# Optimization experiments

Measured on AMD Instinct MI355X. Metric: run time of the kernel, lower is better.

Reference implementation:

```python
import jax, jax.numpy as jnp
import numpy as np

EOS = 1e-10
N = 6000          # nnodes
E = 192000        # n_edges (avg degree 32)
D_IN = 512        # input_dim
H = 128           # hidden_dim
ALPHA = 1.0
TEMP = 1.0
BIAS = 1e-4


def setup_inputs() -> dict:
    key = jax.random.key(0)
    k1, k2, k3, k4, k5, k6, k7 = jax.random.split(key, 7)
    features = jax.random.normal(k1, (N, D_IN), dtype=jnp.float32)
    edges = jax.random.randint(k2, (2, E), 0, N)
    # params: embedding Linear(D_IN->H) and edge MLP Linear(2H->1)
    w_emb = jax.random.normal(k3, (D_IN, H), dtype=jnp.float32) * 0.05
    b_emb = jnp.zeros((H,), jnp.float32)
    w_mlp = jax.random.normal(k4, (2 * H, 1), dtype=jnp.float32) * 0.05
    b_mlp = jnp.zeros((1,), jnp.float32)
    # gumbel-sigmoid noise: eps = (bias-(1-bias))*u + (1-bias)  in [bias, 1-bias]
    u = jax.random.uniform(k5, (E,), dtype=jnp.float32)
    eps = (BIAS - (1.0 - BIAS)) * u + (1.0 - BIAS)
    gate_noise = jnp.log(eps) - jnp.log(1.0 - eps)
    return {"features": features, "edges": edges, "w_emb": w_emb, "b_emb": b_emb,
            "w_mlp": w_mlp, "b_mlp": b_mlp, "gate_noise": gate_noise}


def _normalize_sym(adj):
    d = adj.sum(axis=1)
    inv = 1.0 / (jnp.sqrt(d) + EOS)
    return adj * inv[:, None] * inv[None, :]


def reference(features, edges, w_emb, b_emb, w_mlp, b_mlp, gate_noise):
    # node embeddings: single Linear + ReLU
    emb = jax.nn.relu(features @ w_emb + b_emb)              # [N, H]
    h0 = emb[edges[0]]                                       # [E, H]
    h1 = emb[edges[1]]                                       # [E, H]
    s1 = (jnp.concatenate([h0, h1], axis=1) @ w_mlp + b_mlp).ravel()
    s2 = (jnp.concatenate([h1, h0], axis=1) @ w_mlp + b_mlp).ravel()
    raw = (s1 + s2) * 0.5                                    # [E]
    # gumbel-sigmoid gating
    weights_lp = jax.nn.sigmoid((gate_noise + raw) / TEMP)
    weights_hp = 1.0 - weights_lp

    eye = jnp.eye(N, dtype=features.dtype)

    def build_adj(w):
        adj = jnp.zeros((N, N), features.dtype).at[edges[0], edges[1]].set(w)
        return _normalize_sym(adj + eye)

    adj_lp = build_adj(weights_lp)
    adj_hp = build_adj(weights_hp)
    mask = jnp.zeros((N, N), features.dtype).at[edges[0], edges[1]].set(1.0)
    adj_hp = eye - adj_hp * mask * ALPHA
    adj_unnorm = jnp.zeros((N, N), features.dtype).at[edges[0], edges[1]].set(1.0)
    return (adj_lp, adj_hp, weights_lp, weights_hp, adj_unnorm)
```

## Files before the change

### kernel.cpp

```cpp
#include <hip/hip_runtime.h>
#include <math.h>

#define NNODES 6000
#define NEDGES 192000
#define DIN 512
#define HDIM 128
#define ALPHA 1.0f
#define EOS 1e-10f

static const size_t NN = (size_t)NNODES * (size_t)NNODES;

__global__ __launch_bounds__(128) void embed_g_kernel(
    const float* __restrict__ feat, const float* __restrict__ w_emb,
    const float* __restrict__ b_emb, const float* __restrict__ w_mlp,
    float* __restrict__ g) {
  __shared__ float sf[8 * DIN];
  __shared__ float red[2][8];
  const int t = threadIdx.x;
  const int nb = blockIdx.x * 8;

  const float4* f4 = (const float4*)(feat + (size_t)nb * DIN);
  float4* s4 = (float4*)sf;
#pragma unroll
  for (int k = 0; k < 8; ++k) s4[k * 128 + t] = f4[k * 128 + t];
  __syncthreads();

  const int h = t;
  float acc[8];
  const float b = b_emb[h];
#pragma unroll
  for (int n = 0; n < 8; ++n) acc[n] = b;

#pragma unroll 4
  for (int d = 0; d < DIN; ++d) {
    const float w = w_emb[d * HDIM + h];
#pragma unroll
    for (int n = 0; n < 8; ++n) acc[n] += sf[n * DIN + d] * w;
  }

  const float wv = 0.5f * (w_mlp[h] + w_mlp[HDIM + h]);
  const int lane = t & 63, wave = t >> 6;
#pragma unroll
  for (int n = 0; n < 8; ++n) {
    float v = fmaxf(acc[n], 0.0f) * wv;
    for (int off = 32; off > 0; off >>= 1) v += __shfl_down(v, off, 64);
    if (lane == 0) red[wave][n] = v;
  }
  __syncthreads();
  if (t < 8) g[nb + t] = red[0][t] + red[1][t];
}

__global__ __launch_bounds__(256) void edge_weights_kernel(
    const int* __restrict__ edges, const float* __restrict__ g,
    const float* __restrict__ noise, const float* __restrict__ b_mlp,
    float* __restrict__ w_lp, float* __restrict__ w_hp,
    int* __restrict__ winner) {
  const int e = blockIdx.x * blockDim.x + threadIdx.x;
  if (e >= NEDGES) return;
  const int u = edges[e];
  const int v = edges[NEDGES + e];
  const float raw = g[u] + g[v] + b_mlp[0];
  const float x = noise[e] + raw;
  const float wl = 1.0f / (1.0f + expf(-x));
  const float wh = 1.0f - wl;
  w_lp[e] = wl;
  w_hp[e] = wh;
  atomicMax(&winner[(size_t)u * NNODES + v], e + 1);
}

__global__ __launch_bounds__(256) void edge_deg_kernel(
    const int* __restrict__ edges, const float* __restrict__ w_lp,
    const float* __restrict__ w_hp, const int* __restrict__ winner,
    float* __restrict__ deg_lp, float* __restrict__ deg_hp) {
  const int e = blockIdx.x * blockDim.x + threadIdx.x;
  if (e >= NEDGES) return;
  const int u = edges[e];
  const int v = edges[NEDGES + e];
  if (winner[(size_t)u * NNODES + v] != e + 1) return;
  atomicAdd(&deg_lp[u], w_lp[e]);
  atomicAdd(&deg_hp[u], w_hp[e]);
}

__global__ __launch_bounds__(256) void node_inv_kernel(
    const float* __restrict__ deg_lp, const float* __restrict__ deg_hp,
    float* __restrict__ inv_lp, float* __restrict__ inv_hp,
    float* __restrict__ adj_lp, float* __restrict__ adj_hp) {
  const int i = blockIdx.x * blockDim.x + threadIdx.x;
  if (i >= NNODES) return;
  const float il = 1.0f / (sqrtf(deg_lp[i] + 1.0f) + EOS);
  const float ih = 1.0f / (sqrtf(deg_hp[i] + 1.0f) + EOS);
  inv_lp[i] = il;
  inv_hp[i] = ih;
  const size_t diag = (size_t)i * NNODES + i;
  adj_lp[diag] = il * il;
  adj_hp[diag] = 1.0f;
}

__global__ __launch_bounds__(256) void edge_write_kernel(
    const int* __restrict__ edges, const float* __restrict__ w_lp,
    const float* __restrict__ w_hp, const float* __restrict__ inv_lp,
    const float* __restrict__ inv_hp, float* __restrict__ adj_lp,
    float* __restrict__ adj_hp, float* __restrict__ unnorm) {
  const int e = blockIdx.x * blockDim.x + threadIdx.x;
  if (e >= NEDGES) return;
  const int u = edges[e];
  const int v = edges[NEDGES + e];
  const size_t cell = (size_t)u * NNODES + v;
  const int win = ((const int*)unnorm)[cell];
  if (win != e + 1) return;
  const float wl = w_lp[e];
  const float wh = w_hp[e];
  const float il = inv_lp[u] * inv_lp[v];
  const float ih = inv_hp[u] * inv_hp[v];
  if (u == v) {
    adj_lp[cell] = (wl + 1.0f) * il;
    adj_hp[cell] = 1.0f - (wh + 1.0f) * ih * ALPHA;
  } else {
    adj_lp[cell] = wl * il;
    adj_hp[cell] = -wh * ih * ALPHA;
  }
  unnorm[cell] = 1.0f;
}

extern "C" void kernel_launch(void* const* d_in, const int* in_sizes, int n_in,
                              void* d_out, int out_size, void* d_ws,
                              size_t ws_size, hipStream_t stream) {
  const float* feat  = (const float*)d_in[0];
  const int*   edges = (const int*)d_in[1];
  const float* w_emb = (const float*)d_in[2];
  const float* b_emb = (const float*)d_in[3];
  const float* w_mlp = (const float*)d_in[4];
  const float* b_mlp = (const float*)d_in[5];
  const float* noise = (const float*)d_in[6];

  float* out    = (float*)d_out;
  float* adj_lp = out;
  float* adj_hp = out + NN;
  float* w_lp   = out + 2 * NN;
  float* w_hp   = w_lp + NEDGES;
  float* unnorm = w_hp + NEDGES;

  float* deg_lp = (float*)d_ws;
  float* deg_hp = deg_lp + NNODES;
  float* inv_lp = deg_hp + NNODES;
  float* inv_hp = inv_lp + NNODES;
  float* g      = inv_hp + NNODES;

  hipMemsetAsync(adj_lp, 0, 2 * NN * sizeof(float), stream);
  hipMemsetAsync(unnorm, 0, NN * sizeof(float), stream);
  hipMemsetAsync(deg_lp, 0, 2 * NNODES * sizeof(float), stream);

  embed_g_kernel<<<NNODES / 8, 128, 0, stream>>>(feat, w_emb, b_emb, w_mlp, g);

  const int eb = (NEDGES + 255) / 256;
  edge_weights_kernel<<<eb, 256, 0, stream>>>(edges, g, noise, b_mlp, w_lp,
                                              w_hp, (int*)unnorm);
  edge_deg_kernel<<<eb, 256, 0, stream>>>(edges, w_lp, w_hp,
                                          (const int*)unnorm, deg_lp, deg_hp);
  node_inv_kernel<<<(NNODES + 255) / 256, 256, 0, stream>>>(
      deg_lp, deg_hp, inv_lp, inv_hp, adj_lp, adj_hp);
  edge_write_kernel<<<eb, 256, 0, stream>>>(edges, w_lp, w_hp, inv_lp, inv_hp,
                                            adj_lp, adj_hp, unnorm);
}
```

Baseline: 585.0 us.

## Bucket edges per row and paint dense adjacency rows in one pass

Replaces the full-matrix memsets and scattered per-edge atomics with per-row edge buckets stored in the unnorm buffer. A per-row kernel deduplicates edges in shared memory to compute degrees, and a paint kernel zero-fills each row and scatters its values in one block, removing separate memset traffic. It also vectorizes the shared-memory reads in the embedding GEMV. This assumes row degree stays at or below KMAX and relies on bit-packing edge ids into the scratch output.

```diff
diff --git a/kernel.cpp b/kernel.cpp
--- a/kernel.cpp
+++ b/kernel.cpp
@@ -7,6 +7,7 @@
 #define HDIM 128
 #define ALPHA 1.0f
 #define EOS 1e-10f
+#define KMAX 256
 
 static const size_t NN = (size_t)NNODES * (size_t)NNODES;
 
@@ -31,11 +32,21 @@
 #pragma unroll
   for (int n = 0; n < 8; ++n) acc[n] = b;
 
-#pragma unroll 4
-  for (int d = 0; d < DIN; ++d) {
-    const float w = w_emb[d * HDIM + h];
-#pragma unroll
-    for (int n = 0; n < 8; ++n) acc[n] += sf[n * DIN + d] * w;
+  const float4* sf4 = (const float4*)sf;
+#pragma unroll 2
+  for (int d4 = 0; d4 < DIN / 4; ++d4) {
+    const float w0 = w_emb[(d4 * 4 + 0) * HDIM + h];
+    const float w1 = w_emb[(d4 * 4 + 1) * HDIM + h];
+    const float w2 = w_emb[(d4 * 4 + 2) * HDIM + h];
+    const float w3 = w_emb[(d4 * 4 + 3) * HDIM + h];
+#pragma unroll
+    for (int n = 0; n < 8; ++n) {
+      const float4 f = sf4[n * (DIN / 4) + d4];
+      acc[n] += f.x * w0;
+      acc[n] += f.y * w1;
+      acc[n] += f.z * w2;
+      acc[n] += f.w * w3;
+    }
   }
 
   const float wv = 0.5f * (w_mlp[h] + w_mlp[HDIM + h]);
@@ -50,11 +61,11 @@
   if (t < 8) g[nb + t] = red[0][t] + red[1][t];
 }
 
-__global__ __launch_bounds__(256) void edge_weights_kernel(
+__global__ __launch_bounds__(256) void edge_bucket_kernel(
     const int* __restrict__ edges, const float* __restrict__ g,
     const float* __restrict__ noise, const float* __restrict__ b_mlp,
     float* __restrict__ w_lp, float* __restrict__ w_hp,
-    int* __restrict__ winner) {
+    int* __restrict__ cnt, int* __restrict__ slots) {
   const int e = blockIdx.x * blockDim.x + threadIdx.x;
   if (e >= NEDGES) return;
   const int u = edges[e];
@@ -62,64 +73,150 @@
   const float raw = g[u] + g[v] + b_mlp[0];
   const float x = noise[e] + raw;
   const float wl = 1.0f / (1.0f + expf(-x));
-  const float wh = 1.0f - wl;
   w_lp[e] = wl;
-  w_hp[e] = wh;
-  atomicMax(&winner[(size_t)u * NNODES + v], e + 1);
-}
-
-__global__ __launch_bounds__(256) void edge_deg_kernel(
+  w_hp[e] = 1.0f - wl;
+  const int k = atomicAdd(&cnt[u], 1);
+  if (k < KMAX) slots[(size_t)u * NNODES + k] = e;
+}
+
+__global__ __launch_bounds__(256) void row_dedup_deg_kernel(
     const int* __restrict__ edges, const float* __restrict__ w_lp,
-    const float* __restrict__ w_hp, const int* __restrict__ winner,
-    float* __restrict__ deg_lp, float* __restrict__ deg_hp) {
-  const int e = blockIdx.x * blockDim.x + threadIdx.x;
-  if (e >= NEDGES) return;
-  const int u = edges[e];
-  const int v = edges[NEDGES + e];
-  if (winner[(size_t)u * NNODES + v] != e + 1) return;
-  atomicAdd(&deg_lp[u], w_lp[e]);
-  atomicAdd(&deg_hp[u], w_hp[e]);
+    const float* __restrict__ w_hp, const int* __restrict__ cnt,
+    int* __restrict__ slots, float* __restrict__ deg_lp,
+    float* __restrict__ deg_hp) {
+  __shared__ int se[4][KMAX];
+  __shared__ int sv[4][KMAX];
+  __shared__ float sl[4][KMAX];
+  __shared__ float sh[4][KMAX];
+  const int wid = threadIdx.x >> 6;
+  const int lane = threadIdx.x & 63;
+  const int r = blockIdx.x * 4 + wid;
+
+  int k = cnt[r];
+  if (k > KMAX) k = KMAX;
+  int* srow = slots + (size_t)r * NNODES;
+  for (int i = lane; i < k; i += 64) {
+    const int e = srow[i];
+    se[wid][i] = e;
+    sv[wid][i] = edges[NEDGES + e];
+    sl[wid][i] = w_lp[e];
+    sh[wid][i] = w_hp[e];
+  }
+  __syncthreads();
+
+  float suml = 0.0f, sumh = 0.0f;
+  for (int i = lane; i < k; i += 64) {
+    const int e = se[wid][i];
+    const int v = sv[wid][i];
+    int win = 1;
+    for (int j = 0; j < k; ++j) {
+      if (sv[wid][j] == v && se[wid][j] > e) { win = 0; break; }
+    }
+    if (win) {
+      suml += sl[wid][i];
+      sumh += sh[wid][i];
+    }
+    srow[i] = (e << 14) | (v << 1) | win;
+  }
+  for (int off = 32; off > 0; off >>= 1) {
+    suml += __shfl_down(suml, off, 64);
+    sumh += __shfl_down(sumh, off, 64);
+  }
+  if (lane == 0) {
+    deg_lp[r] = suml;
+    deg_hp[r] = sumh;
+  }
 }
 
 __global__ __launch_bounds__(256) void node_inv_kernel(
     const float* __restrict__ deg_lp, const float* __restrict__ deg_hp,
-    float* __restrict__ inv_lp, float* __restrict__ inv_hp,
-    float* __restrict__ adj_lp, float* __restrict__ adj_hp) {
+    float* __restrict__ inv_lp, float* __restrict__ inv_hp) {
   const int i = blockIdx.x * blockDim.x + threadIdx.x;
   if (i >= NNODES) return;
-  const float il = 1.0f / (sqrtf(deg_lp[i] + 1.0f) + EOS);
-  const float ih = 1.0f / (sqrtf(deg_hp[i] + 1.0f) + EOS);
-  inv_lp[i] = il;
-  inv_hp[i] = ih;
-  const size_t diag = (size_t)i * NNODES + i;
-  adj_lp[diag] = il * il;
-  adj_hp[diag] = 1.0f;
-}
-
-__global__ __launch_bounds__(256) void edge_write_kernel(
-    const int* __restrict__ edges, const float* __restrict__ w_lp,
-    const float* __restrict__ w_hp, const float* __restrict__ inv_lp,
-    const float* __restrict__ inv_hp, float* __restrict__ adj_lp,
+  inv_lp[i] = 1.0f / (sqrtf(deg_lp[i] + 1.0f) + EOS);
+  inv_hp[i] = 1.0f / (sqrtf(deg_hp[i] + 1.0f) + EOS);
+}
+
+__global__ __launch_bounds__(256) void paint_kernel(
+    const float* __restrict__ w_lp, const float* __restrict__ w_hp,
+    const float* __restrict__ inv_lp, const float* __restrict__ inv_hp,
+    const int* __restrict__ cnt, float* __restrict__ adj_lp,
     float* __restrict__ adj_hp, float* __restrict__ unnorm) {
-  const int e = blockIdx.x * blockDim.x + threadIdx.x;
-  if (e >= NEDGES) return;
-  const int u = edges[e];
-  const int v = edges[NEDGES + e];
-  const size_t cell = (size_t)u * NNODES + v;
-  const int win = ((const int*)unnorm)[cell];
-  if (win != e + 1) return;
-  const float wl = w_lp[e];
-  const float wh = w_hp[e];
-  const float il = inv_lp[u] * inv_lp[v];
-  const float ih = inv_hp[u] * inv_hp[v];
-  if (u == v) {
-    adj_lp[cell] = (wl + 1.0f) * il;
-    adj_hp[cell] = 1.0f - (wh + 1.0f) * ih * ALPHA;
-  } else {
-    adj_lp[cell] = wl * il;
-    adj_hp[cell] = -wh * ih * ALPHA;
-  }
-  unnorm[cell] = 1.0f;
+  __shared__ int scol[KMAX];
+  __shared__ float slp[KMAX];
+  __shared__ float shp[KMAX];
+  __shared__ int has_self;
+  __shared__ float sdiag[2];
+
+  const int t = threadIdx.x;
+  const int r = blockIdx.x;
+  int k = cnt[r];
+  if (k > KMAX) k = KMAX;
+  const float il = inv_lp[r];
+  const float ih = inv_hp[r];
+
+  float* lp_row = adj_lp + (size_t)r * NNODES;
+  float* hp_row = adj_hp + (size_t)r * NNODES;
+  float* un_row = unnorm + (size_t)r * NNODES;
+  const int* srow = (const int*)un_row;
+
+  if (t == 0) {
+    has_self = 0;
+    sdiag[0] = 0.0f;
+    sdiag[1] = 0.0f;
+  }
+  __syncthreads();
+
+  if (t < k) {
+    const int raw = srow[t];
+    const int win = raw & 1;
+    const int v = (raw >> 1) & 0x1FFF;
+    const int e = (int)(((unsigned)raw) >> 14);
+    const float wl = w_lp[e];
+    const float wh = w_hp[e];
+    scol[t] = (v << 1) | win;
+    slp[t] = wl * il * inv_lp[v];
+    shp[t] = -ALPHA * wh * ih * inv_hp[v];
+    if (v == r) {
+      has_self = 1;
+      if (win) {
+        sdiag[0] = wl;
+        sdiag[1] = wh;
+      }
+    }
+  }
+  __syncthreads();
+
+  const float4 z = make_float4(0.0f, 0.0f, 0.0f, 0.0f);
+  float4* lp4 = (float4*)lp_row;
+  float4* hp4 = (float4*)hp_row;
+  float4* un4 = (float4*)un_row;
+  for (int c = t; c < NNODES / 4; c += 256) {
+    lp4[c] = z;
+    hp4[c] = z;
+    un4[c] = z;
+  }
+  __syncthreads();
+
+  if (t < k) {
+    const int cw = scol[t];
+    const int win = cw & 1;
+    const int v = cw >> 1;
+    un_row[v] = 1.0f;
+    if (win && v != r) {
+      lp_row[v] = slp[t];
+      hp_row[v] = shp[t];
+    }
+  }
+  if (t == 0) {
+    if (has_self) {
+      lp_row[r] = (sdiag[0] + 1.0f) * il * il;
+      hp_row[r] = 1.0f - (sdiag[1] + 1.0f) * ih * ih * ALPHA;
+    } else {
+      lp_row[r] = il * il;
+      hp_row[r] = 1.0f;
+    }
+  }
 }
 
 extern "C" void kernel_launch(void* const* d_in, const int* in_sizes, int n_in,
@@ -140,25 +237,26 @@
   float* w_hp   = w_lp + NEDGES;
   float* unnorm = w_hp + NEDGES;
 
-  float* deg_lp = (float*)d_ws;
+  float* g      = (float*)d_ws;
+  float* deg_lp = g + NNODES;
   float* deg_hp = deg_lp + NNODES;
   float* inv_lp = deg_hp + NNODES;
   float* inv_hp = inv_lp + NNODES;
-  float* g      = inv_hp + NNODES;
-
-  hipMemsetAsync(adj_lp, 0, 2 * NN * sizeof(float), stream);
-  hipMemsetAsync(unnorm, 0, NN * sizeof(float), stream);
-  hipMemsetAsync(deg_lp, 0, 2 * NNODES * sizeof(float), stream);
+  int*   cnt    = (int*)(inv_hp + NNODES);
+
+  hipMemsetAsync(cnt, 0, NNODES * sizeof(int), stream);
 
   embed_g_kernel<<<NNODES / 8, 128, 0, stream>>>(feat, w_emb, b_emb, w_mlp, g);
 
-  const int eb = (NEDGES + 255) / 256;
-  edge_weights_kernel<<<eb, 256, 0, stream>>>(edges, g, noise, b_mlp, w_lp,
-                                              w_hp, (int*)unnorm);
-  edge_deg_kernel<<<eb, 256, 0, stream>>>(edges, w_lp, w_hp,
-                                          (const int*)unnorm, deg_lp, deg_hp);
+  edge_bucket_kernel<<<NEDGES / 256, 256, 0, stream>>>(
+      edges, g, noise, b_mlp, w_lp, w_hp, cnt, (int*)unnorm);
+
+  row_dedup_deg_kernel<<<NNODES / 4, 256, 0, stream>>>(
+      edges, w_lp, w_hp, cnt, (int*)unnorm, deg_lp, deg_hp);
+
   node_inv_kernel<<<(NNODES + 255) / 256, 256, 0, stream>>>(
-      deg_lp, deg_hp, inv_lp, inv_hp, adj_lp, adj_hp);
-  edge_write_kernel<<<eb, 256, 0, stream>>>(edges, w_lp, w_hp, inv_lp, inv_hp,
-                                            adj_lp, adj_hp, unnorm);
-}
+      deg_lp, deg_hp, inv_lp, inv_hp);
+
+  paint_kernel<<<NNODES, 256, 0, stream>>>(w_lp, w_hp, inv_lp, inv_hp, cnt,
+                                           adj_lp, adj_hp, unnorm);
+}
```

After: 530.2 us. 9.4% less time.
